# Performance work log

Measured on AMD Instinct MI355X. Metric: run time of the kernel, lower is better.

The kernel has to match this reference:

```python
import jax, jax.numpy as jnp
import numpy as np

N, E, D0, D1, H = 20000, 640000, 64, 32, 64


def setup_inputs() -> dict:
    key = jax.random.key(0)
    ks = jax.random.split(key, 16)
    s = 0.1
    return {
        'feat0e': jax.random.normal(ks[0], (N, D0), jnp.float32),
        'feat1o': jax.random.normal(ks[1], (N, D1, 3), jnp.float32),
        'edge_attr': jax.random.normal(ks[2], (E, H), jnp.float32),
        'pos': jax.random.normal(ks[3], (N, 3), jnp.float32),
        'edge_index': jax.random.randint(ks[4], (2, E), 0, N, jnp.int64),
        # edge_net: FullyConnectedNet([H]*3 -> [H]) with silu
        'W1': jax.random.normal(ks[5], (H, H), jnp.float32) * s,
        'b1': jnp.zeros((H,), jnp.float32),
        'W2': jax.random.normal(ks[6], (H, H), jnp.float32) * s,
        'b2': jnp.zeros((H,), jnp.float32),
        'W3': jax.random.normal(ks[7], (H, H), jnp.float32) * s,
        'b3': jnp.zeros((H,), jnp.float32),
        # tensor-product path weights (internal weights, not shared)
        'w_ss': jax.random.normal(ks[8], (D0, H, D0), jnp.float32) * s,     # 0e x 0e -> 0e
        'w_vv': jax.random.normal(ks[9], (D1, D0), jnp.float32) * s,        # 1o . 1o -> 0e
        'w_sv': jax.random.normal(ks[10], (D0, D1), jnp.float32) * s,       # 0e x 1o -> 1o
        'w_vs': jax.random.normal(ks[11], (D1, H, D1), jnp.float32) * s,    # 1o x 0e -> 1o
        'w_cross': jax.random.normal(ks[12], (D1, D1), jnp.float32) * s,    # 1o x 1o -> 1o (cross)
        # gate: scalars -> per-vector-channel gates
        'Wg': jax.random.normal(ks[13], (D0, D1), jnp.float32) * s,
        'bg': jnp.zeros((D1,), jnp.float32),
    }


def reference(feat0e, feat1o, edge_attr, pos, edge_index,
              W1, b1, W2, b2, W3, b3,
              w_ss, w_vv, w_sv, w_vs, w_cross, Wg, bg):
    src, dst = edge_index[0], edge_index[1]

    # edge MLP (silu)
    h = jax.nn.silu(edge_attr @ W1 + b1)
    h = jax.nn.silu(h @ W2 + b2)
    edge_scalar = h @ W3 + b3                      # [E, H]

    rel_pos = pos[dst] - pos[src]                  # [E, 3]
    s_src = feat0e[src]                            # [E, D0]
    v_src = feat1o[src]                            # [E, D1, 3]

    # equivariant tensor product per edge
    dot_vv = jnp.sum(v_src * rel_pos[:, None, :], axis=-1)          # [E, D1]
    msg0e = (jnp.einsum('ep,eh,pho->eo', s_src, edge_scalar, w_ss)
             + dot_vv @ w_vv)                                        # [E, D0]
    cross_vv = jnp.cross(v_src, rel_pos[:, None, :])                 # [E, D1, 3]
    msg1o = (jnp.einsum('ep,pc,ex->ecx', s_src, w_sv, rel_pos)
             + jnp.einsum('edx,eh,dhc->ecx', v_src, edge_scalar, w_vs)
             + jnp.einsum('edx,dc->ecx', cross_vv, w_cross))          # [E, D1, 3]

    # scatter_mean over destination nodes
    counts = jax.ops.segment_sum(jnp.ones((E,), msg0e.dtype), dst, num_segments=N)
    denom = jnp.maximum(counts, 1.0)
    aggr0e = jax.ops.segment_sum(msg0e, dst, num_segments=N) / denom[:, None]
    aggr1o = jax.ops.segment_sum(msg1o, dst, num_segments=N) / denom[:, None, None]

    # gate + residual
    out0e = jax.nn.silu(aggr0e) + feat0e                              # [N, D0]
    gates = jax.nn.silu(aggr0e @ Wg + bg)                             # [N, D1]
    out1o = aggr1o * gates[:, :, None] + feat1o                       # [N, D1, 3]

    # concat flattened outputs into one array [N, D0 + 3*D1]
    return jnp.concatenate([out0e, out1o.reshape(N, D1 * 3)], axis=-1)
```

## Files before the change

### kernel.cpp

```cpp
#include <hip/hip_runtime.h>


#define NN 20000
#define EE 640000
#define D0 64
#define D1 32
#define HH 64

typedef _Float16 half8 __attribute__((ext_vector_type(8)));
typedef _Float16 half4 __attribute__((ext_vector_type(4)));
typedef float f32x4 __attribute__((ext_vector_type(4)));

__device__ __forceinline__ float silu_f(float x) { return x / (1.0f + __expf(-x)); }
__device__ __forceinline__ _Float16 u2h(unsigned short u) {
    union { unsigned short u; _Float16 h; } c; c.u = u; return c.h;
}
__device__ __forceinline__ unsigned short h2u(_Float16 h) {
    union { unsigned short u; _Float16 h; } c; c.h = h; return c.u;
}
__device__ __forceinline__ half8 pack8(float4 a, float4 b) {
    half8 h;
    h[0]=(_Float16)a.x; h[1]=(_Float16)a.y; h[2]=(_Float16)a.z; h[3]=(_Float16)a.w;
    h[4]=(_Float16)b.x; h[5]=(_Float16)b.y; h[6]=(_Float16)b.z; h[7]=(_Float16)b.w;
    return h;
}

#define OFF_HIST  0ull
#define OFF_RS    81920ull
#define OFF_CUR   163840ull
#define OFF_FLAG  245760ull
#define OFF_SRCA  262144ull
#define OFF_DSTA  2822144ull
#define OFF_PE    5382144ull
#define OFF_WSS   7942144ull
#define OFF_WVS2  8466432ull
#define OFF_WVV   8597504ull
#define OFF_WSV   8601600ull
#define OFF_WX    8605696ull
#define OFF_WMLP  8607744ull
#define OFF_MSG   8632320ull
#define WS_NEED   (8632320ull + 122880000ull)

__global__ void detect_idx_kernel(const int* __restrict__ eidx, int* __restrict__ flag) {
    int odd_nz = 0, even_nz = 0;
    for (int k = 0; k < 64; ++k) {
        if (eidx[2 * k + 1] != 0) odd_nz = 1;
        if (eidx[2 * k] != 0) even_nz = 1;
    }
    *flag = (!odd_nz && even_nz) ? 1 : 0;
}

__global__ __launch_bounds__(256) void hist_kernel(
    const int* __restrict__ eidx, const int* __restrict__ flag,
    int* __restrict__ hist)
{
    const int e = blockIdx.x * 256 + threadIdx.x;
    int d_;
    if (*flag) d_ = (int)((const long long*)eidx)[EE + e];
    else       d_ = eidx[EE + e];
    atomicAdd(hist + d_, 1);
}

__global__ __launch_bounds__(1024) void scan_kernel(
    const int* __restrict__ hist, int* __restrict__ rs, int* __restrict__ cur)
{
    __shared__ int part[1024];
    const int t = threadIdx.x;
    const int base = t * 20;
    int loc[20];
    int tot = 0;
#pragma unroll
    for (int k = 0; k < 20; ++k) {
        int n = base + k;
        int h = (n < NN) ? hist[n] : 0;
        loc[k] = tot; tot += h;
    }
    part[t] = tot;
    __syncthreads();
    for (int off = 1; off < 1024; off <<= 1) {
        int v = (t >= off) ? part[t - off] : 0;
        __syncthreads();
        part[t] += v;
        __syncthreads();
    }
    int excl = part[t] - tot;
#pragma unroll
    for (int k = 0; k < 20; ++k) {
        int n = base + k;
        if (n < NN) { rs[n] = excl + loc[k]; cur[n] = excl + loc[k]; }
    }
    if (t == 1023) rs[NN] = part[1023];
}

__global__ __launch_bounds__(256) void scatter_kernel(
    const int* __restrict__ eidx, const int* __restrict__ flag,
    int* __restrict__ cur, int* __restrict__ srca, int* __restrict__ dsta,
    int* __restrict__ pe)
{
    const int e = blockIdx.x * 256 + threadIdx.x;
    int s_, d_;
    if (*flag) { s_ = (int)((const long long*)eidx)[e]; d_ = (int)((const long long*)eidx)[EE + e]; }
    else       { s_ = eidx[e];                          d_ = eidx[EE + e]; }
    int pos = atomicAdd(cur + d_, 1);
    srca[pos] = s_; dsta[pos] = d_; pe[pos] = e;
}

__global__ __launch_bounds__(256) void prep_kernel(
    const float* __restrict__ wss, const float* __restrict__ wvv,
    const float* __restrict__ wsv, const float* __restrict__ wvs,
    const float* __restrict__ wx,
    const float* __restrict__ W1, const float* __restrict__ W2,
    const float* __restrict__ W3, char* __restrict__ ws)
{
    int id = blockIdx.x * 256 + threadIdx.x;
    if (id >= 43136) return;
    int l = id & 63;
    int l4 = l >> 4, l16 = l & 15;
    half8 o;
    _Float16* dst;
    if (id < 32768) {
        int p = id >> 9; int frag = (id >> 6) & 7;
        int kf = frag >> 2, nf = frag & 3;
#pragma unroll
        for (int j = 0; j < 8; j++) {
            int h = kf * 32 + l4 * 8 + j, oo = nf * 16 + l16;
            o[j] = (_Float16)wss[((size_t)p * 64 + h) * 64 + oo];
        }
        dst = (_Float16*)(ws + OFF_WSS) + (size_t)id * 8;
    } else if (id < 40960) {
        int i = id - 32768;
        int f = i >> 6;
        int chunk = f >> 3, kf = (f >> 2) & 1, nfl = f & 3;
#pragma unroll
        for (int j = 0; j < 8; j++) {
            int h = kf * 32 + l4 * 8 + j;
            int col = chunk * 64 + nfl * 16 + l16;
            int d = col >> 5, c = col & 31;
            o[j] = (_Float16)wvs[((size_t)d * 64 + h) * 32 + c];
        }
        dst = (_Float16*)(ws + OFF_WVS2) + (size_t)i * 8;
    } else if (id < 41216) {
        int i = id - 40960; int nf = i >> 6;
#pragma unroll
        for (int j = 0; j < 8; j++) {
            int d = l4 * 8 + j, oo = nf * 16 + l16;
            o[j] = (_Float16)wvv[d * 64 + oo];
        }
        dst = (_Float16*)(ws + OFF_WVV) + (size_t)i * 8;
    } else if (id < 41472) {
        int i = id - 41216; int frag = i >> 6;
        int kf = frag >> 1, nf = frag & 1;
#pragma unroll
        for (int j = 0; j < 8; j++) {
            int p = kf * 32 + l4 * 8 + j, c = nf * 16 + l16;
            o[j] = (_Float16)wsv[p * 32 + c];
        }
        dst = (_Float16*)(ws + OFF_WSV) + (size_t)i * 8;
    } else if (id < 41600) {
        int i = id - 41472; int nf = i >> 6;
#pragma unroll
        for (int j = 0; j < 8; j++) {
            int d = l4 * 8 + j, c = nf * 16 + l16;
            o[j] = (_Float16)wx[d * 32 + c];
        }
        dst = (_Float16*)(ws + OFF_WX) + (size_t)i * 8;
    } else {
        int i = id - 41600; int f = i >> 6;
        int layer = f >> 3, kf = (f >> 2) & 1, nf = f & 3;
        const float* W = layer == 0 ? W1 : (layer == 1 ? W2 : W3);
#pragma unroll
        for (int j = 0; j < 8; j++) {
            int r = kf * 32 + l4 * 8 + j, cc = nf * 16 + l16;
            o[j] = (_Float16)W[r * 64 + cc];
        }
        dst = (_Float16*)(ws + OFF_WMLP) + (size_t)i * 8;
    }
    *(half8*)dst = o;
}

__device__ __forceinline__ void mlp_wave(
    const float* __restrict__ edge_attr,
    const float* __restrict__ b1, const float* __restrict__ b2,
    const float* __restrict__ b3,
    const char* __restrict__ wsp,
    const int* __restrict__ pel_w,
    unsigned short* __restrict__ xch,
    int lane, half8 esf[4][2])
{
    const int l4 = lane >> 4, l16 = lane & 15;
    const half8* wm = (const half8*)(wsp + OFF_WMLP);

    float bias[3][4];
#pragma unroll
    for (int nf = 0; nf < 4; nf++) {
        bias[0][nf] = b1[nf * 16 + l16];
        bias[1][nf] = b2[nf * 16 + l16];
        bias[2][nf] = b3[nf * 16 + l16];
    }

    half8 af[4][2];
#pragma unroll
    for (int mf = 0; mf < 4; mf++) {
        int e = pel_w[mf * 16 + l16];
        const float* p = edge_attr + (size_t)e * 64 + l4 * 8;
#pragma unroll
        for (int kf = 0; kf < 2; kf++)
            af[mf][kf] = pack8(*(const float4*)(p + kf * 32),
                               *(const float4*)(p + kf * 32 + 4));
    }

#pragma unroll
    for (int layer = 0; layer < 3; ++layer) {
        f32x4 acc[4][4];
#pragma unroll
        for (int mf = 0; mf < 4; mf++)
#pragma unroll
            for (int nf = 0; nf < 4; nf++) acc[mf][nf] = (f32x4){0.f,0.f,0.f,0.f};
#pragma unroll
        for (int kf = 0; kf < 2; kf++)
#pragma unroll
            for (int mf = 0; mf < 4; mf++)
#pragma unroll
                for (int nf = 0; nf < 4; nf++)
                    acc[mf][nf] = __builtin_amdgcn_mfma_f32_16x16x32_f16(
                        af[mf][kf], wm[(layer * 8 + kf * 4 + nf) * 64 + lane],
                        acc[mf][nf], 0, 0, 0);
#pragma unroll
        for (int mf = 0; mf < 4; mf++)
#pragma unroll
            for (int nf = 0; nf < 4; nf++)
#pragma unroll
                for (int reg = 0; reg < 4; reg++) {
                    int row = mf * 16 + l4 * 4 + reg;
                    int col = nf * 16 + l16;
                    float v = acc[mf][nf][reg] + bias[layer][nf];
                    if (layer < 2) v = silu_f(v);
                    xch[row * 64 + (col ^ ((row & 7) << 3))] = h2u((_Float16)v);
                }
        if (layer < 2) {
#pragma unroll
            for (int mf = 0; mf < 4; mf++)
#pragma unroll
                for (int kf = 0; kf < 2; kf++) {
                    int row = mf * 16 + l16;
                    int cs = kf * 32 + l4 * 8;
                    af[mf][kf] = *(const half8*)&xch[row * 64 + (cs ^ ((row & 7) << 3))];
                }
        }
    }
#pragma unroll
    for (int mf = 0; mf < 4; mf++)
#pragma unroll
        for (int kf = 0; kf < 2; kf++) {
            int row = mf * 16 + l16;
            int cs = kf * 32 + l4 * 8;
            esf[mf][kf] = *(const half8*)&xch[row * 64 + (cs ^ ((row & 7) << 3))];
        }
}

__global__ __launch_bounds__(256, 2) void msg0e_kernel(
    const float* __restrict__ feat0e,
    const float* __restrict__ feat1o,
    const float* __restrict__ edge_attr,
    const float* __restrict__ pos,
    const float* __restrict__ b1, const float* __restrict__ b2,
    const float* __restrict__ b3,
    const char* __restrict__ wsp,
    _Float16* __restrict__ msg0)
{
    __shared__ unsigned short st[4][4096];
    __shared__ unsigned short wf[16384];
    __shared__ float rell[4][64][3];
    __shared__ int   srcl[4][64];
    __shared__ int   pel[4][64];

    const int tid = threadIdx.x, w = tid >> 6, lane = tid & 63;
    const int l4 = lane >> 4, l16 = lane & 15;
    const long i0 = (long)blockIdx.x * 256 + w * 64;

    {
        long p = i0 + lane;
        int s_ = ((const int*)(wsp + OFF_SRCA))[p];
        int d_ = ((const int*)(wsp + OFF_DSTA))[p];
        pel[w][lane] = ((const int*)(wsp + OFF_PE))[p];
        srcl[w][lane] = s_;
        rell[w][lane][0] = pos[d_ * 3 + 0] - pos[s_ * 3 + 0];
        rell[w][lane][1] = pos[d_ * 3 + 1] - pos[s_ * 3 + 1];
        rell[w][lane][2] = pos[d_ * 3 + 2] - pos[s_ * 3 + 2];
    }
    __syncthreads();

    half8 esf[4][2];
    mlp_wave(edge_attr, b1, b2, b3, wsp, pel[w], st[w], lane, esf);
    __syncthreads();

#pragma unroll
    for (int r4 = 0; r4 < 4; r4++) {
        int row = r4 * 16 + (lane >> 2);
        int ch = lane & 3;
        const float* sp = feat0e + (size_t)srcl[w][row] * 64 + ch * 16;
        half8 h0 = pack8(*(const float4*)(sp + 0), *(const float4*)(sp + 4));
        half8 h1 = pack8(*(const float4*)(sp + 8), *(const float4*)(sp + 12));
        int r7 = row & 7;
        *(half8*)&st[w][row * 64 + (((ch * 2) ^ r7) * 8)]     = h0;
        *(half8*)&st[w][row * 64 + (((ch * 2 + 1) ^ r7) * 8)] = h1;
    }
    __syncthreads();

    f32x4 acc[4][4];
#pragma unroll
    for (int mf = 0; mf < 4; mf++)
#pragma unroll
        for (int nf = 0; nf < 4; nf++) acc[mf][nf] = (f32x4){0.f, 0.f, 0.f, 0.f};

    const half8* wss_g = (const half8*)(wsp + OFF_WSS);
    half8* wfh = (half8*)wf;
    for (int pc = 0; pc < 16; ++pc) {
        __syncthreads();
#pragma unroll
        for (int q = 0; q < 8; q++)
            wfh[q * 256 + tid] = wss_g[pc * 2048 + q * 256 + tid];
        __syncthreads();
#pragma unroll
        for (int pl = 0; pl < 4; ++pl) {
            const int p = pc * 4 + pl;
            _Float16 sv[4];
#pragma unroll
            for (int mf = 0; mf < 4; mf++) {
                int row = mf * 16 + l16;
                sv[mf] = u2h(st[w][row * 64 + (((p >> 3) ^ (row & 7)) * 8) + (p & 7)]);
            }
#pragma unroll
            for (int kf = 0; kf < 2; kf++) {
                half8 bf[4];
#pragma unroll
                for (int nf = 0; nf < 4; nf++)
                    bf[nf] = wfh[(pl * 8 + kf * 4 + nf) * 64 + lane];
#pragma unroll
                for (int mf = 0; mf < 4; mf++) {
                    half8 a = esf[mf][kf] * sv[mf];
#pragma unroll
                    for (int nf = 0; nf < 4; nf++)
                        acc[mf][nf] = __builtin_amdgcn_mfma_f32_16x16x32_f16(a, bf[nf], acc[mf][nf], 0, 0, 0);
// ... 151 lines not shown
                bsv[kf][nf] = wsvp[(size_t)(kf * 2 + nf) * 64 + lane];
#pragma unroll
        for (int g = 0; g < 4; g++) {
            int erow = g * 16 + l16;
            const float* sp = feat0e + (size_t)srcl[w][erow] * 64 + l4 * 8;
            half8 sf[2];
#pragma unroll
            for (int kf = 0; kf < 2; kf++)
                sf[kf] = pack8(*(const float4*)(sp + kf * 32),
                               *(const float4*)(sp + kf * 32 + 4));
#pragma unroll
            for (int x = 0; x < 3; x++) {
                _Float16 rl = (_Float16)rell[w][erow][x];
#pragma unroll
                for (int kf = 0; kf < 2; kf++) {
                    half8 a = sf[kf] * rl;
#pragma unroll
                    for (int nf = 0; nf < 2; nf++)
                        acc1[g][x][nf] = __builtin_amdgcn_mfma_f32_16x16x32_f16(
                            a, bsv[kf][nf], acc1[g][x][nf], 0, 0, 0);
                }
            }
        }
    }

    {
        half8 bx[2];
        bx[0] = wxp[lane];
        bx[1] = wxp[64 + lane];
#pragma unroll
        for (int g = 0; g < 4; g++) {
            f32x4 cx[3][2];
#pragma unroll
            for (int xp = 0; xp < 3; xp++) {
                half8 av;
#pragma unroll
                for (int j = 0; j < 8; j++)
                    av[j] = u2h(vt[w][((l4 * 8 + j) * 3 + xp) * 64 + g * 16 + l16]);
#pragma unroll
                for (int nf = 0; nf < 2; nf++)
                    cx[xp][nf] = __builtin_amdgcn_mfma_f32_16x16x32_f16(
                        av, bx[nf], (f32x4){0.f,0.f,0.f,0.f}, 0, 0, 0);
            }
            f32x4 r[3];
#pragma unroll
            for (int x = 0; x < 3; x++)
#pragma unroll
                for (int reg = 0; reg < 4; reg++)
                    r[x][reg] = rell[w][g * 16 + l4 * 4 + reg][x];
#pragma unroll
            for (int x = 0; x < 3; x++) {
                const int x1 = (x + 1) % 3, x2 = (x + 2) % 3;
#pragma unroll
                for (int ch = 0; ch < 2; ch++)
                    acc1[g][x][ch] += r[x2] * cx[x1][ch] - r[x1] * cx[x2][ch];
            }
        }
    }

    __syncthreads();
#pragma unroll
    for (int g = 0; g < 4; g++)
#pragma unroll
        for (int reg = 0; reg < 4; reg++) {
            int row = g * 16 + l4 * 4 + reg;
            int sw = (row & 3) << 3;
#pragma unroll
            for (int x = 0; x < 3; x++)
#pragma unroll
                for (int ch = 0; ch < 2; ch++) {
                    int c32 = ch * 16 + l16;
                    vt[w][row * 96 + x * 32 + (c32 ^ sw)] = h2u((_Float16)acc1[g][x][ch][reg]);
                }
        }
#pragma unroll
    for (int tt = 0; tt < 12; tt++) {
        int x = tt >> 2, rem = (tt & 3) * 8;
        int col = x * 32 + (rem ^ ((lane & 3) << 3));
        half8 v = *(const half8*)&vt[w][lane * 96 + col];
        *(half8*)(msg1 + (size_t)(i0 + lane) * 96 + tt * 8) = v;
    }
}

__global__ __launch_bounds__(256) void gather0_kernel(
    const float* __restrict__ feat0e,
    const float* __restrict__ Wg, const float* __restrict__ bg,
    const char* __restrict__ wsp, const _Float16* __restrict__ msg0,
    float* __restrict__ out)
{
    __shared__ float Wgl[2048];
    __shared__ float ag[4][64];
    const int tid = threadIdx.x, w = tid >> 6, lane = tid & 63;
    for (int t = tid; t < 2048; t += 256) Wgl[t] = Wg[t];

    const int n = blockIdx.x * 4 + w;
    const int* rs = (const int*)(wsp + OFF_RS);
    const int i0 = rs[n], i1 = rs[n + 1];
    const int r8 = lane >> 3, c8 = lane & 7;

    float a[8];
#pragma unroll
    for (int j = 0; j < 8; j++) a[j] = 0.f;
    for (int i = i0 + r8; i < i1; i += 8) {
        half8 m = *(const half8*)(msg0 + (size_t)i * 64 + c8 * 8);
#pragma unroll
        for (int j = 0; j < 8; j++) a[j] += (float)m[j];
    }
#pragma unroll
    for (int s = 8; s < 64; s <<= 1)
#pragma unroll
        for (int j = 0; j < 8; j++) a[j] += __shfl_xor(a[j], s);
    if (r8 == 0)
#pragma unroll
        for (int j = 0; j < 8; j++) ag[w][c8 * 8 + j] = a[j];
    __syncthreads();

    const float inv = 1.0f / fmaxf((float)(i1 - i0), 1.0f);
    float av = ag[w][lane] * inv;
    out[(size_t)n * 160 + lane] = silu_f(av) + feat0e[(size_t)n * 64 + lane];

    if (lane < 32) {
        float gs = bg[lane];
#pragma unroll
        for (int p = 0; p < 64; ++p) gs = fmaf(ag[w][p] * inv, Wgl[p * 32 + lane], gs);
        out[(size_t)n * 160 + 64 + lane] = silu_f(gs);
    }
}

__global__ __launch_bounds__(256) void gather1_kernel(
    const float* __restrict__ feat1o,
    const char* __restrict__ wsp, const _Float16* __restrict__ msg1,
    float* __restrict__ out)
{
    __shared__ float ag1[4][96];
    __shared__ float gl[4][32];
    const int tid = threadIdx.x, w = tid >> 6, lane = tid & 63;
    const int n = blockIdx.x * 4 + w;
    const int* rs = (const int*)(wsp + OFF_RS);
    const int i0 = rs[n], i1 = rs[n + 1];

    if (lane < 32) gl[w][lane] = out[(size_t)n * 160 + 64 + lane];

    const int r4 = lane >> 4, c12 = lane & 15;
    float a[8];
#pragma unroll
    for (int j = 0; j < 8; j++) a[j] = 0.f;
    if (c12 < 12)
        for (int i = i0 + r4; i < i1; i += 4) {
            half8 m = *(const half8*)(msg1 + (size_t)i * 96 + c12 * 8);
#pragma unroll
            for (int j = 0; j < 8; j++) a[j] += (float)m[j];
        }
#pragma unroll
    for (int s = 16; s < 64; s <<= 1)
#pragma unroll
        for (int j = 0; j < 8; j++) a[j] += __shfl_xor(a[j], s);
    if (r4 == 0 && c12 < 12)
#pragma unroll
        for (int j = 0; j < 8; j++) ag1[w][c12 * 8 + j] = a[j];
    __syncthreads();

    const float inv = 1.0f / fmaxf((float)(i1 - i0), 1.0f);
#pragma unroll
    for (int t = 0; t < 2; t++) {
        int idx = t * 64 + lane;
        if (idx < 96) {
            int c = idx / 3, x = idx - 3 * c;
            float v = ag1[w][x * 32 + c] * inv * gl[w][c] + feat1o[(size_t)n * 96 + idx];
            out[(size_t)n * 160 + 64 + idx] = v;
        }
    }
}

__global__ __launch_bounds__(256) void edge_kernel_fb(
    const float* __restrict__ feat0e, const float* __restrict__ feat1o,
    const float* __restrict__ edge_attr, const float* __restrict__ pos,
    const int* __restrict__ eidx,
    const float* __restrict__ W1, const float* __restrict__ b1,
    const float* __restrict__ W2, const float* __restrict__ b2,
    const float* __restrict__ W3, const float* __restrict__ b3,
    const float* __restrict__ wss, const float* __restrict__ wvv,
    const float* __restrict__ wsv, const float* __restrict__ wvs,
    const float* __restrict__ wcross,
    const int* __restrict__ i64flag,
    float* __restrict__ out, float* __restrict__ counts)
{
    const int e = blockIdx.x * 256 + threadIdx.x;
    int src, dst;
    if (*i64flag) { src = (int)((const long long*)eidx)[e]; dst = (int)((const long long*)eidx)[EE + e]; }
    else          { src = eidx[e];                          dst = eidx[EE + e]; }
    const float rel0 = pos[dst * 3 + 0] - pos[src * 3 + 0];
    const float rel1 = pos[dst * 3 + 1] - pos[src * 3 + 1];
    const float rel2 = pos[dst * 3 + 2] - pos[src * 3 + 2];
    float h1[HH];
#pragma unroll
    for (int j = 0; j < HH; ++j) h1[j] = b1[j];
    for (int i = 0; i < HH; ++i) {
        float a = edge_attr[(size_t)e * HH + i];
        const float* ww = W1 + i * HH;
#pragma unroll
        for (int j = 0; j < HH; ++j) h1[j] = fmaf(a, ww[j], h1[j]);
    }
#pragma unroll
    for (int j = 0; j < HH; ++j) h1[j] = silu_f(h1[j]);
    float h2[HH];
#pragma unroll
    for (int j = 0; j < HH; ++j) h2[j] = b2[j];
#pragma unroll
    for (int i = 0; i < HH; ++i) {
        float a = h1[i];
        const float* ww = W2 + i * HH;
#pragma unroll
        for (int j = 0; j < HH; ++j) h2[j] = fmaf(a, ww[j], h2[j]);
    }
#pragma unroll
    for (int j = 0; j < HH; ++j) h2[j] = silu_f(h2[j]);
    float es[HH];
#pragma unroll
    for (int j = 0; j < HH; ++j) es[j] = b3[j];
#pragma unroll
    for (int i = 0; i < HH; ++i) {
        float a = h2[i];
        const float* ww = W3 + i * HH;
#pragma unroll
        for (int j = 0; j < HH; ++j) es[j] = fmaf(a, ww[j], es[j]);
    }
    float dotv[D1];
#pragma unroll
    for (int d = 0; d < D1; ++d) {
        float v0 = feat1o[(size_t)src * 96 + d * 3 + 0];
        float v1 = feat1o[(size_t)src * 96 + d * 3 + 1];
        float v2 = feat1o[(size_t)src * 96 + d * 3 + 2];
        dotv[d] = fmaf(v0, rel0, fmaf(v1, rel1, v2 * rel2));
    }
#pragma unroll
    for (int ob = 0; ob < 4; ++ob) {
        const int o0 = ob * 16;
        float acc[16];
#pragma unroll
        for (int j = 0; j < 16; ++j) acc[j] = 0.f;
#pragma unroll
        for (int d = 0; d < D1; ++d) {
            const float* ww = wvv + d * D0 + o0;
#pragma unroll
            for (int j = 0; j < 16; ++j) acc[j] = fmaf(dotv[d], ww[j], acc[j]);
        }
        for (int p = 0; p < D0; ++p) {
            float sval = feat0e[(size_t)src * D0 + p];
            const float* wp = wss + (size_t)p * HH * D0 + o0;
#pragma unroll
            for (int h = 0; h < HH; ++h) {
                float c = sval * es[h];
                const float* ww = wp + h * D0;
#pragma unroll
                for (int j = 0; j < 16; ++j) acc[j] = fmaf(c, ww[j], acc[j]);
            }
        }
        float* obase = out + (size_t)dst * 160 + o0;
#pragma unroll
        for (int j = 0; j < 16; ++j) atomicAdd(obase + j, acc[j]);
    }
    atomicAdd(counts + dst, 1.0f);
    float g[D1];
#pragma unroll
    for (int c = 0; c < D1; ++c) g[c] = 0.f;
    for (int p = 0; p < D0; ++p) {
        float sval = feat0e[(size_t)src * D0 + p];
        const float* ww = wsv + p * D1;
#pragma unroll
        for (int c = 0; c < D1; ++c) g[c] = fmaf(sval, ww[c], g[c]);
    }
    float acc1[D1 * 3];
#pragma unroll
    for (int c = 0; c < D1; ++c) {
        acc1[c * 3 + 0] = g[c] * rel0;
        acc1[c * 3 + 1] = g[c] * rel1;
        acc1[c * 3 + 2] = g[c] * rel2;
    }
    for (int d = 0; d < D1; ++d) {
        float v0 = feat1o[(size_t)src * 96 + d * 3 + 0];
        float v1 = feat1o[(size_t)src * 96 + d * 3 + 1];
        float v2 = feat1o[(size_t)src * 96 + d * 3 + 2];
        float cx0 = fmaf(v1, rel2, -v2 * rel1);
        float cx1 = fmaf(v2, rel0, -v0 * rel2);
        float cx2 = fmaf(v0, rel1, -v1 * rel0);
        const float* wd = wvs + (size_t)d * HH * D1;
        const float* wc = wcross + d * D1;
#pragma unroll
        for (int cb = 0; cb < 2; ++cb) {
            float t[16];
#pragma unroll
            for (int cc = 0; cc < 16; ++cc) t[cc] = 0.f;
#pragma unroll
            for (int h = 0; h < HH; ++h) {
                const float* ww = wd + h * D1 + cb * 16;
                float ev = es[h];
#pragma unroll
                for (int cc = 0; cc < 16; ++cc) t[cc] = fmaf(ev, ww[cc], t[cc]);
            }
#pragma unroll
            for (int cc = 0; cc < 16; ++cc) {
                int c = cb * 16 + cc;
                float tc = t[cc], wcc = wc[c];
                acc1[c * 3 + 0] = fmaf(v0, tc, fmaf(cx0, wcc, acc1[c * 3 + 0]));
                acc1[c * 3 + 1] = fmaf(v1, tc, fmaf(cx1, wcc, acc1[c * 3 + 1]));
                acc1[c * 3 + 2] = fmaf(v2, tc, fmaf(cx2, wcc, acc1[c * 3 + 2]));
            }
        }
    }
    float* obase1 = out + (size_t)dst * 160 + 64;
#pragma unroll
    for (int k = 0; k < D1 * 3; ++k) atomicAdd(obase1 + k, acc1[k]);
}

__global__ __launch_bounds__(256) void node_kernel_fb(
    const float* __restrict__ feat0e,
    const float* __restrict__ feat1o,
    const float* __restrict__ Wg, const float* __restrict__ bg,
    const float* __restrict__ counts,
    float* __restrict__ out)
{
    const int w = threadIdx.x >> 6;
    const int n = blockIdx.x * 4 + w;
    const int lane = threadIdx.x & 63;
    __shared__ float a_lds[4][D0];
    __shared__ float gate_lds[4][D1];

    const float inv = 1.0f / fmaxf(counts[n], 1.0f);
    float a = out[(size_t)n * 160 + lane] * inv;
    a_lds[w][lane] = a;
    __syncthreads();

    out[(size_t)n * 160 + lane] = silu_f(a) + feat0e[(size_t)n * D0 + lane];

    if (lane < D1) {
        float gs = bg[lane];
        for (int p = 0; p < D0; ++p) gs = fmaf(a_lds[w][p], Wg[p * D1 + lane], gs);
        gate_lds[w][lane] = silu_f(gs);
    }
    __syncthreads();

    for (int idx = lane; idx < D1 * 3; idx += 64) {
        int c = idx / 3;
        size_t o = (size_t)n * 160 + 64 + idx;
        out[o] = fmaf(out[o] * inv, gate_lds[w][c], feat1o[(size_t)n * (D1 * 3) + idx]);
    }
}

extern "C" void kernel_launch(void* const* d_in, const int* in_sizes, int n_in,
                              void* d_out, int out_size, void* d_ws, size_t ws_size,
                              hipStream_t stream) {
    const float* feat0e    = (const float*)d_in[0];
    const float* feat1o    = (const float*)d_in[1];
    const float* edge_attr = (const float*)d_in[2];
    const float* pos       = (const float*)d_in[3];
    const int*   eidx      = (const int*)d_in[4];
    const float* W1 = (const float*)d_in[5];
    const float* b1 = (const float*)d_in[6];
    const float* W2 = (const float*)d_in[7];
    const float* b2 = (const float*)d_in[8];
    const float* W3 = (const float*)d_in[9];
    const float* b3 = (const float*)d_in[10];
    const float* wss    = (const float*)d_in[11];
    const float* wvv    = (const float*)d_in[12];
    const float* wsv    = (const float*)d_in[13];
    const float* wvs    = (const float*)d_in[14];
    const float* wcross = (const float*)d_in[15];
    const float* Wg = (const float*)d_in[16];
    const float* bg = (const float*)d_in[17];

    float* out = (float*)d_out;
    char*  ws  = (char*)d_ws;
    int* hist = (int*)(ws + OFF_HIST);
    int* rs   = (int*)(ws + OFF_RS);
    int* cur  = (int*)(ws + OFF_CUR);
    int* flag = (int*)(ws + OFF_FLAG);

    detect_idx_kernel<<<1, 1, 0, stream>>>(eidx, flag);

    if (ws_size >= WS_NEED) {
        int* srca = (int*)(ws + OFF_SRCA);
        int* dsta = (int*)(ws + OFF_DSTA);
        int* pe   = (int*)(ws + OFF_PE);
        _Float16* msg = (_Float16*)(ws + OFF_MSG);

        hipMemsetAsync(ws + OFF_HIST, 0, NN * sizeof(int), stream);
        hist_kernel<<<EE / 256, 256, 0, stream>>>(eidx, flag, hist);
        scan_kernel<<<1, 1024, 0, stream>>>(hist, rs, cur);
        scatter_kernel<<<EE / 256, 256, 0, stream>>>(eidx, flag, cur, srca, dsta, pe);
        prep_kernel<<<169, 256, 0, stream>>>(wss, wvv, wsv, wvs, wcross, W1, W2, W3, ws);

        msg0e_kernel<<<EE / 256, 256, 0, stream>>>(
            feat0e, feat1o, edge_attr, pos, b1, b2, b3, (const char*)ws, msg);
        gather0_kernel<<<NN / 4, 256, 0, stream>>>(
            feat0e, Wg, bg, (const char*)ws, msg, out);
        msg1o_kernel<<<EE / 256, 256, 0, stream>>>(
            feat0e, feat1o, edge_attr, pos, b1, b2, b3, (const char*)ws, msg);
        gather1_kernel<<<NN / 4, 256, 0, stream>>>(
            feat1o, (const char*)ws, msg, out);
    } else {
        float* counts = (float*)(ws + OFF_HIST);
        hipMemsetAsync(d_out, 0, (size_t)out_size * sizeof(float), stream);
        hipMemsetAsync(ws + OFF_HIST, 0, NN * sizeof(float), stream);
        edge_kernel_fb<<<EE / 256, 256, 0, stream>>>(
            feat0e, feat1o, edge_attr, pos, eidx,
            W1, b1, W2, b2, W3, b3, wss, wvv, wsv, wvs, wcross,
            flag, out, counts);
        node_kernel_fb<<<NN / 4, 256, 0, stream>>>(feat0e, feat1o, Wg, bg, counts, out);
    }
}
```

Measured before the change: 767.6 us.

## Precompute per-source tensor-product weights and process edges grouped by source

Edges are re-sorted by source node and padded to 16-edge tiles. Each tile then shares one source, so the per-node tensor feat0e·w_ss (64×64 fp16) can be computed once per node in a new gG kernel. The msg0e kernel now needs only an edge_scalar × G[src] matmul instead of the full three-way contraction, which cuts per-edge MFMA work by roughly the D0 factor. In exchange it adds extra sort/scatter passes, a large G buffer with chunked fallback, padded rows in the edge MLP, and an indirect map lookup in gather0.

```diff
diff --git a/kernel.cpp b/kernel.cpp
--- a/kernel.cpp
+++ b/kernel.cpp
@@ -6,6 +6,8 @@
 #define D0 64
 #define D1 32
 #define HH 64
+#define EPMAX 940032
+#define NTILES 58752
 
 typedef _Float16 half8 __attribute__((ext_vector_type(8)));
 typedef _Float16 half4 __attribute__((ext_vector_type(4)));
@@ -29,6 +31,7 @@
 #define OFF_RS    81920ull
 #define OFF_CUR   163840ull
 #define OFF_FLAG  245760ull
+#define OFF_EPT   245764ull
 #define OFF_SRCA  262144ull
 #define OFF_DSTA  2822144ull
 #define OFF_PE    5382144ull
@@ -39,7 +42,18 @@
 #define OFF_WX    8605696ull
 #define OFF_WMLP  8607744ull
 #define OFF_MSG   8632320ull
-#define WS_NEED   (8632320ull + 122880000ull)
+#define WS_R4_NEED 131512320ull
+#define OFF_WSSG  131512320ull
+#define OFF_OUTD  132036608ull
+#define OFF_PSP   132118528ull
+#define OFF_CURS  132200448ull
+#define OFF_SRCT  132282368ull
+#define OFF_POSOF 132528128ull
+#define OFF_MAP   135088128ull
+#define OFF_DSTP  137648128ull
+#define OFF_PEP   141408256ull
+#define OFF_G     145168384ull
+#define NEED_S(npp) (OFF_G + (unsigned long long)(npp) * 8192ull)
 
 __global__ void detect_idx_kernel(const int* __restrict__ eidx, int* __restrict__ flag) {
     int odd_nz = 0, even_nz = 0;
@@ -50,15 +64,28 @@
     *flag = (!odd_nz && even_nz) ? 1 : 0;
 }
 
+__device__ __forceinline__ void load_sd(const int* eidx, const int* flag, int e,
+                                        int& s_, int& d_) {
+    if (*flag) { s_ = (int)((const long long*)eidx)[e]; d_ = (int)((const long long*)eidx)[EE + e]; }
+    else       { s_ = eidx[e];                          d_ = eidx[EE + e]; }
+}
+
 __global__ __launch_bounds__(256) void hist_kernel(
+    const int* __restrict__ eidx, const int* __restrict__ flag, int* __restrict__ hist)
+{
+    const int e = blockIdx.x * 256 + threadIdx.x;
+    int s_, d_; load_sd(eidx, flag, e, s_, d_);
+    atomicAdd(hist + d_, 1);
+}
+
+__global__ __launch_bounds__(256) void hist2_kernel(
     const int* __restrict__ eidx, const int* __restrict__ flag,
-    int* __restrict__ hist)
+    int* __restrict__ hist, int* __restrict__ outd)
 {
     const int e = blockIdx.x * 256 + threadIdx.x;
-    int d_;
-    if (*flag) d_ = (int)((const long long*)eidx)[EE + e];
-    else       d_ = eidx[EE + e];
+    int s_, d_; load_sd(eidx, flag, e, s_, d_);
     atomicAdd(hist + d_, 1);
+    atomicAdd(outd + s_, 1);
 }
 
 __global__ __launch_bounds__(1024) void scan_kernel(
@@ -92,15 +119,80 @@
     if (t == 1023) rs[NN] = part[1023];
 }
 
-__global__ __launch_bounds__(256) void scatter_kernel(
+__global__ __launch_bounds__(1024) void scanP_kernel(
+    const int* __restrict__ outd, int* __restrict__ psP, int* __restrict__ curS,
+    int* __restrict__ srcT, int* __restrict__ epT)
+{
+    __shared__ int part[1024];
+    const int t = threadIdx.x;
+    const int base = t * 20;
+    int loc[20];
+    int tot = 0;
+#pragma unroll
+    for (int k = 0; k < 20; ++k) {
+        int n = base + k;
+        int p = (n < NN) ? ((outd[n] + 15) & ~15) : 0;
+        loc[k] = tot; tot += p;
+    }
+    part[t] = tot;
+    __syncthreads();
+    for (int off = 1; off < 1024; off <<= 1) {
+        int v = (t >= off) ? part[t - off] : 0;
+        __syncthreads();
+        part[t] += v;
+        __syncthreads();
+    }
+    int excl = part[t] - tot;
+#pragma unroll
+    for (int k = 0; k < 20; ++k) {
+        int n = base + k;
+        if (n < NN) {
+            int start = excl + loc[k];
+            psP[n] = start; curS[n] = start;
+            int p = (outd[n] + 15) & ~15;
+            for (int tt = start >> 4; tt < (start + p) >> 4; ++tt) srcT[tt] = n;
+        }
+    }
+    if (t == 1023) *epT = part[1023] >> 4;
+}
+
+__global__ __launch_bounds__(256) void fillpad_kernel(
+    const int* __restrict__ epT, int* __restrict__ srcT)
+{
+    int t = blockIdx.x * 256 + threadIdx.x;
+    if (t < NTILES && t >= *epT) srcT[t] = NN;
+}
+
+__global__ __launch_bounds__(256) void srcscat_kernel(
+    const int* __restrict__ eidx, const int* __restrict__ flag,
+    int* __restrict__ curS, int* __restrict__ dstP, int* __restrict__ peP,
+    int* __restrict__ posof)
+{
+    const int e = blockIdx.x * 256 + threadIdx.x;
+    int s_, d_; load_sd(eidx, flag, e, s_, d_);
+    int pos = atomicAdd(curS + s_, 1);
+    dstP[pos] = d_; peP[pos] = e; posof[e] = pos;
+}
+
+__global__ __launch_bounds__(256) void dstscat2_kernel(
+    const int* __restrict__ eidx, const int* __restrict__ flag,
+    int* __restrict__ cur, int* __restrict__ srca, int* __restrict__ dsta,
+    int* __restrict__ pe, const int* __restrict__ posof, int* __restrict__ map)
+{
+    const int e = blockIdx.x * 256 + threadIdx.x;
+    int s_, d_; load_sd(eidx, flag, e, s_, d_);
+    int j = atomicAdd(cur + d_, 1);
+    srca[j] = s_; dsta[j] = d_; pe[j] = e;
+    if (map) map[j] = posof[e];
+}
+
+__global__ __launch_bounds__(256) void scatter_r4_kernel(
     const int* __restrict__ eidx, const int* __restrict__ flag,
     int* __restrict__ cur, int* __restrict__ srca, int* __restrict__ dsta,
     int* __restrict__ pe)
 {
     const int e = blockIdx.x * 256 + threadIdx.x;
-    int s_, d_;
-    if (*flag) { s_ = (int)((const long long*)eidx)[e]; d_ = (int)((const long long*)eidx)[EE + e]; }
-    else       { s_ = eidx[e];                          d_ = eidx[EE + e]; }
+    int s_, d_; load_sd(eidx, flag, e, s_, d_);
     int pos = atomicAdd(cur + d_, 1);
     srca[pos] = s_; dsta[pos] = d_; pe[pos] = e;
 }
@@ -110,10 +202,10 @@
     const float* __restrict__ wsv, const float* __restrict__ wvs,
     const float* __restrict__ wx,
     const float* __restrict__ W1, const float* __restrict__ W2,
-    const float* __restrict__ W3, char* __restrict__ ws)
+    const float* __restrict__ W3, char* __restrict__ ws, int maxid)
 {
     int id = blockIdx.x * 256 + threadIdx.x;
-    if (id >= 43136) return;
+    if (id >= maxid) return;
     int l = id & 63;
     int l4 = l >> 4, l16 = l & 15;
     half8 o;
@@ -164,7 +256,7 @@
             o[j] = (_Float16)wx[d * 32 + c];
         }
         dst = (_Float16*)(ws + OFF_WX) + (size_t)i * 8;
-    } else {
+    } else if (id < 43136) {
         int i = id - 41600; int f = i >> 6;
         int layer = f >> 3, kf = (f >> 2) & 1, nf = f & 3;
         const float* W = layer == 0 ? W1 : (layer == 1 ? W2 : W3);
@@ -174,8 +266,62 @@
             o[j] = (_Float16)W[r * 64 + cc];
         }
         dst = (_Float16*)(ws + OFF_WMLP) + (size_t)i * 8;
+    } else {
+        int i = id - 43136;
+        int f = i >> 6;
+        int q = f >> 3, kfp = (f >> 2) & 1, nfp = f & 3;
+#pragma unroll
+        for (int j = 0; j < 8; j++) {
+            int p = kfp * 32 + l4 * 8 + j;
+            int cc = q * 64 + nfp * 16 + l16;
+            int jc = cc & 7, lc = (cc >> 3) & 63, fi = cc >> 9;
+            int kfc = fi >> 2, nfc = fi & 3;
+            int h = kfc * 32 + (lc >> 4) * 8 + jc;
+            int oo = nfc * 16 + (lc & 15);
+            o[j] = (_Float16)wss[((size_t)p * 64 + h) * 64 + oo];
+        }
+        dst = (_Float16*)(ws + OFF_WSSG) + (size_t)i * 8;
     }
     *(half8*)dst = o;
+}
+
+__global__ __launch_bounds__(256, 2) void gG_kernel(
+    const float* __restrict__ feat0e, const char* __restrict__ wsp,
+    int lo, int hi, _Float16* __restrict__ G)
+{
+    const int tid = threadIdx.x, w = tid >> 6, lane = tid & 63;
+    const int l4 = lane >> 4, l16 = lane & 15;
+    const int n0 = lo + blockIdx.x * 64 + w * 16;
+    if (n0 >= hi) return;
+
+    half8 af[2];
+    {
+        int n = n0 + l16; if (n >= NN) n = NN - 1;
+        const float* sp = feat0e + (size_t)n * 64 + l4 * 8;
+        af[0] = pack8(*(const float4*)sp, *(const float4*)(sp + 4));
+        af[1] = pack8(*(const float4*)(sp + 32), *(const float4*)(sp + 36));
+    }
+    const half8* wg = (const half8*)(wsp + OFF_WSSG);
+    for (int q = 0; q < 64; ++q) {
+        f32x4 acc[4];
+#pragma unroll
+        for (int nf = 0; nf < 4; nf++) acc[nf] = (f32x4){0.f,0.f,0.f,0.f};
+#pragma unroll
+        for (int kf = 0; kf < 2; kf++)
+#pragma unroll
+            for (int nf = 0; nf < 4; nf++)
+                acc[nf] = __builtin_amdgcn_mfma_f32_16x16x32_f16(
+                    af[kf], wg[(q * 8 + kf * 4 + nf) * 64 + lane], acc[nf], 0, 0, 0);
+#pragma unroll
+        for (int nf = 0; nf < 4; nf++)
+#pragma unroll
+            for (int reg = 0; reg < 4; reg++) {
+                int n = n0 + l4 * 4 + reg;
+                if (n < hi && n < NN)
+                    G[(size_t)(n - lo) * 4096 + q * 64 + nf * 16 + l16] =
+                        (_Float16)acc[nf][reg];
+            }
+    }
 }
 
 __device__ __forceinline__ void mlp_wave(
@@ -258,7 +404,120 @@
         }
 }
 
-__global__ __launch_bounds__(256, 2) void msg0e_kernel(
+__global__ __launch_bounds__(256, 4) void msg0e_big_kernel(
+    const float* __restrict__ feat1o,
+    const float* __restrict__ edge_attr,
+    const float* __restrict__ pos,
+    const float* __restrict__ b1, const float* __restrict__ b2,
+    const float* __restrict__ b3,
+    const char* __restrict__ wsp,
+    const _Float16* __restrict__ G,
+    int lo, int hi,
+    _Float16* __restrict__ msg0)
+{
+    __shared__ unsigned short st[4][4096];
+    __shared__ float rell[4][64][3];
+    __shared__ int pel[4][64];
+
+    const int tid = threadIdx.x, w = tid >> 6, lane = tid & 63;
+    const int l4 = lane >> 4, l16 = lane & 15;
+    const int i0 = blockIdx.x * 256 + w * 64;
+    const int t0 = i0 >> 4;
+
+    const int* srcT = (const int*)(wsp + OFF_SRCT);
+    int sm[4]; bool act[4]; bool any = false;
+#pragma unroll
+    for (int mf = 0; mf < 4; mf++) {
+        sm[mf] = srcT[t0 + mf];
+        act[mf] = (sm[mf] >= lo && sm[mf] < hi);
+        any = any || act[mf];
+    }
+    if (!any) return;
+
+    {
+        int row = i0 + lane;
+        int my_s = sm[l4];
+        int s_ld = my_s < NN ? my_s : 0;
+        int d_ = ((const int*)(wsp + OFF_DSTP))[row];
+        pel[w][lane] = ((const int*)(wsp + OFF_PEP))[row];
+        rell[w][lane][0] = pos[d_ * 3 + 0] - pos[s_ld * 3 + 0];
+        rell[w][lane][1] = pos[d_ * 3 + 1] - pos[s_ld * 3 + 1];
+        rell[w][lane][2] = pos[d_ * 3 + 2] - pos[s_ld * 3 + 2];
+    }
+
+    half8 esf[4][2];
+    mlp_wave(edge_attr, b1, b2, b3, wsp, pel[w], st[w], lane, esf);
+
+    f32x4 acc[4][4];
+#pragma unroll
+    for (int mf = 0; mf < 4; mf++)
+#pragma unroll
+        for (int nf = 0; nf < 4; nf++) acc[mf][nf] = (f32x4){0.f, 0.f, 0.f, 0.f};
+
+    const half8* Gb = (const half8*)G;
+#pragma unroll
+    for (int mf = 0; mf < 4; mf++) {
+        if (!act[mf]) continue;
+        const half8* gn = Gb + (size_t)(sm[mf] - lo) * 512;
+#pragma unroll
+        for (int kf = 0; kf < 2; kf++)
+#pragma unroll
+            for (int nf = 0; nf < 4; nf++) {
+                half8 bf = gn[(kf * 4 + nf) * 64 + lane];
+                acc[mf][nf] = __builtin_amdgcn_mfma_f32_16x16x32_f16(
+                    esf[mf][kf], bf, acc[mf][nf], 0, 0, 0);
+            }
+    }
+
+    const half8* wvvp = (const half8*)(wsp + OFF_WVV);
+#pragma unroll
+    for (int mf = 0; mf < 4; mf++) {
+        if (!act[mf]) continue;
+        int row = mf * 16 + l16;
+        float r0 = rell[w][row][0], r1 = rell[w][row][1], r2 = rell[w][row][2];
+        const float* vp = feat1o + (size_t)sm[mf] * 96 + l4 * 24;
+        float4 A = *(const float4*)(vp + 0),  B = *(const float4*)(vp + 4);
+        float4 C = *(const float4*)(vp + 8),  D = *(const float4*)(vp + 12);
+        float4 E = *(const float4*)(vp + 16), F = *(const float4*)(vp + 20);
+        half8 dvf;
+        dvf[0] = (_Float16)(A.x * r0 + A.y * r1 + A.z * r2);
+        dvf[1] = (_Float16)(A.w * r0 + B.x * r1 + B.y * r2);
+        dvf[2] = (_Float16)(B.z * r0 + B.w * r1 + C.x * r2);
+        dvf[3] = (_Float16)(C.y * r0 + C.z * r1 + C.w * r2);
+        dvf[4] = (_Float16)(D.x * r0 + D.y * r1 + D.z * r2);
+        dvf[5] = (_Float16)(D.w * r0 + E.x * r1 + E.y * r2);
+        dvf[6] = (_Float16)(E.z * r0 + E.w * r1 + F.x * r2);
+        dvf[7] = (_Float16)(F.y * r0 + F.z * r1 + F.w * r2);
+#pragma unroll
+        for (int nf = 0; nf < 4; nf++)
+            acc[mf][nf] = __builtin_amdgcn_mfma_f32_16x16x32_f16(
+                dvf, wvvp[nf * 64 + lane], acc[mf][nf], 0, 0, 0);
+    }
+
+#pragma unroll
+    for (int mf = 0; mf < 4; mf++) {
+        if (!act[mf]) continue;
+#pragma unroll
+        for (int nf = 0; nf < 4; nf++)
+#pragma unroll
+            for (int reg = 0; reg < 4; reg++) {
+                int row = mf * 16 + l4 * 4 + reg;
+                int col = nf * 16 + l16;
+                st[w][row * 64 + (col ^ ((row & 7) << 3))] =
+                    h2u((_Float16)acc[mf][nf][reg]);
+            }
+    }
+#pragma unroll
+    for (int t = 0; t < 8; t++) {
+        if (!act[t >> 1]) continue;
+        int row = t * 8 + (lane >> 3);
+        int c8 = lane & 7;
+        half8 v = *(const half8*)&st[w][row * 64 + ((c8 * 8) ^ ((row & 7) << 3))];
+        *(half8*)(msg0 + (size_t)(i0 + row) * 64 + c8 * 8) = v;
+    }
+}
+
+__global__ __launch_bounds__(256, 2) void msg0e_r4_kernel(
     const float* __restrict__ feat0e,
     const float* __restrict__ feat1o,
     const float* __restrict__ edge_attr,
@@ -576,7 +835,7 @@
     }
 }
 
-__global__ __launch_bounds__(256) void gather0_kernel(
+__global__ __launch_bounds__(256) void gather0_r4_kernel(
     const float* __restrict__ feat0e,
     const float* __restrict__ Wg, const float* __restrict__ bg,
     const char* __restrict__ wsp, const _Float16* __restrict__ msg0,
@@ -597,6 +856,53 @@
     for (int j = 0; j < 8; j++) a[j] = 0.f;
     for (int i = i0 + r8; i < i1; i += 8) {
         half8 m = *(const half8*)(msg0 + (size_t)i * 64 + c8 * 8);
+#pragma unroll
+        for (int j = 0; j < 8; j++) a[j] += (float)m[j];
+    }
+#pragma unroll
+    for (int s = 8; s < 64; s <<= 1)
+#pragma unroll
+        for (int j = 0; j < 8; j++) a[j] += __shfl_xor(a[j], s);
+    if (r8 == 0)
+#pragma unroll
+        for (int j = 0; j < 8; j++) ag[w][c8 * 8 + j] = a[j];
+    __syncthreads();
+
+    const float inv = 1.0f / fmaxf((float)(i1 - i0), 1.0f);
+    float av = ag[w][lane] * inv;
+    out[(size_t)n * 160 + lane] = silu_f(av) + feat0e[(size_t)n * 64 + lane];
+
+    if (lane < 32) {
+        float gs = bg[lane];
+#pragma unroll
+        for (int p = 0; p < 64; ++p) gs = fmaf(ag[w][p] * inv, Wgl[p * 32 + lane], gs);
+        out[(size_t)n * 160 + 64 + lane] = silu_f(gs);
+    }
+}
+
+__global__ __launch_bounds__(256) void gather0_big_kernel(
+    const float* __restrict__ feat0e,
+    const float* __restrict__ Wg, const float* __restrict__ bg,
+    const char* __restrict__ wsp, const _Float16* __restrict__ msg0,
+    float* __restrict__ out)
+{
+    __shared__ float Wgl[2048];
+    __shared__ float ag[4][64];
+    const int tid = threadIdx.x, w = tid >> 6, lane = tid & 63;
+    for (int t = tid; t < 2048; t += 256) Wgl[t] = Wg[t];
+
+    const int n = blockIdx.x * 4 + w;
+    const int* rs = (const int*)(wsp + OFF_RS);
+    const int* map = (const int*)(wsp + OFF_MAP);
+    const int i0 = rs[n], i1 = rs[n + 1];
+    const int r8 = lane >> 3, c8 = lane & 7;
+
+    float a[8];
+#pragma unroll
+    for (int j = 0; j < 8; j++) a[j] = 0.f;
+    for (int i = i0 + r8; i < i1; i += 8) {
+        int row = map[i];
+        half8 m = *(const half8*)(msg0 + (size_t)row * 64 + c8 * 8);
 #pragma unroll
         for (int j = 0; j < 8; j++) a[j] += (float)m[j];
     }
@@ -663,181 +969,6 @@
             float v = ag1[w][x * 32 + c] * inv * gl[w][c] + feat1o[(size_t)n * 96 + idx];
             out[(size_t)n * 160 + 64 + idx] = v;
         }
-    }
-}
-
-__global__ __launch_bounds__(256) void edge_kernel_fb(
-    const float* __restrict__ feat0e, const float* __restrict__ feat1o,
-    const float* __restrict__ edge_attr, const float* __restrict__ pos,
-    const int* __restrict__ eidx,
-    const float* __restrict__ W1, const float* __restrict__ b1,
-    const float* __restrict__ W2, const float* __restrict__ b2,
-    const float* __restrict__ W3, const float* __restrict__ b3,
-    const float* __restrict__ wss, const float* __restrict__ wvv,
-    const float* __restrict__ wsv, const float* __restrict__ wvs,
-    const float* __restrict__ wcross,
-    const int* __restrict__ i64flag,
-    float* __restrict__ out, float* __restrict__ counts)
-{
-    const int e = blockIdx.x * 256 + threadIdx.x;
-    int src, dst;
-    if (*i64flag) { src = (int)((const long long*)eidx)[e]; dst = (int)((const long long*)eidx)[EE + e]; }
-    else          { src = eidx[e];                          dst = eidx[EE + e]; }
-    const float rel0 = pos[dst * 3 + 0] - pos[src * 3 + 0];
-    const float rel1 = pos[dst * 3 + 1] - pos[src * 3 + 1];
-    const float rel2 = pos[dst * 3 + 2] - pos[src * 3 + 2];
-    float h1[HH];
-#pragma unroll
-    for (int j = 0; j < HH; ++j) h1[j] = b1[j];
-    for (int i = 0; i < HH; ++i) {
-        float a = edge_attr[(size_t)e * HH + i];
-        const float* ww = W1 + i * HH;
-#pragma unroll
-        for (int j = 0; j < HH; ++j) h1[j] = fmaf(a, ww[j], h1[j]);
-    }
-#pragma unroll
-    for (int j = 0; j < HH; ++j) h1[j] = silu_f(h1[j]);
-    float h2[HH];
-#pragma unroll
-    for (int j = 0; j < HH; ++j) h2[j] = b2[j];
-#pragma unroll
-    for (int i = 0; i < HH; ++i) {
-        float a = h1[i];
-        const float* ww = W2 + i * HH;
-#pragma unroll
-        for (int j = 0; j < HH; ++j) h2[j] = fmaf(a, ww[j], h2[j]);
-    }
-#pragma unroll
-    for (int j = 0; j < HH; ++j) h2[j] = silu_f(h2[j]);
-    float es[HH];
-#pragma unroll
-    for (int j = 0; j < HH; ++j) es[j] = b3[j];
-#pragma unroll
-    for (int i = 0; i < HH; ++i) {
-        float a = h2[i];
-        const float* ww = W3 + i * HH;
-#pragma unroll
-        for (int j = 0; j < HH; ++j) es[j] = fmaf(a, ww[j], es[j]);
-    }
-    float dotv[D1];
-#pragma unroll
-    for (int d = 0; d < D1; ++d) {
-        float v0 = feat1o[(size_t)src * 96 + d * 3 + 0];
-        float v1 = feat1o[(size_t)src * 96 + d * 3 + 1];
-        float v2 = feat1o[(size_t)src * 96 + d * 3 + 2];
-        dotv[d] = fmaf(v0, rel0, fmaf(v1, rel1, v2 * rel2));
-    }
-#pragma unroll
-    for (int ob = 0; ob < 4; ++ob) {
-        const int o0 = ob * 16;
-        float acc[16];
-#pragma unroll
-        for (int j = 0; j < 16; ++j) acc[j] = 0.f;
-#pragma unroll
-        for (int d = 0; d < D1; ++d) {
-            const float* ww = wvv + d * D0 + o0;
-#pragma unroll
-            for (int j = 0; j < 16; ++j) acc[j] = fmaf(dotv[d], ww[j], acc[j]);
-        }
-        for (int p = 0; p < D0; ++p) {
-            float sval = feat0e[(size_t)src * D0 + p];
-            const float* wp = wss + (size_t)p * HH * D0 + o0;
-#pragma unroll
-            for (int h = 0; h < HH; ++h) {
-                float c = sval * es[h];
-                const float* ww = wp + h * D0;
-#pragma unroll
-                for (int j = 0; j < 16; ++j) acc[j] = fmaf(c, ww[j], acc[j]);
-            }
-        }
-        float* obase = out + (size_t)dst * 160 + o0;
-#pragma unroll
-        for (int j = 0; j < 16; ++j) atomicAdd(obase + j, acc[j]);
-    }
-    atomicAdd(counts + dst, 1.0f);
-    float g[D1];
-#pragma unroll
-    for (int c = 0; c < D1; ++c) g[c] = 0.f;
-    for (int p = 0; p < D0; ++p) {
-        float sval = feat0e[(size_t)src * D0 + p];
-        const float* ww = wsv + p * D1;
-#pragma unroll
-        for (int c = 0; c < D1; ++c) g[c] = fmaf(sval, ww[c], g[c]);
-    }
-    float acc1[D1 * 3];
-#pragma unroll
-    for (int c = 0; c < D1; ++c) {
-        acc1[c * 3 + 0] = g[c] * rel0;
-        acc1[c * 3 + 1] = g[c] * rel1;
-        acc1[c * 3 + 2] = g[c] * rel2;
-    }
-    for (int d = 0; d < D1; ++d) {
-        float v0 = feat1o[(size_t)src * 96 + d * 3 + 0];
-        float v1 = feat1o[(size_t)src * 96 + d * 3 + 1];
-        float v2 = feat1o[(size_t)src * 96 + d * 3 + 2];
-        float cx0 = fmaf(v1, rel2, -v2 * rel1);
-        float cx1 = fmaf(v2, rel0, -v0 * rel2);
-        float cx2 = fmaf(v0, rel1, -v1 * rel0);
-        const float* wd = wvs + (size_t)d * HH * D1;
-        const float* wc = wcross + d * D1;
-#pragma unroll
-        for (int cb = 0; cb < 2; ++cb) {
-            float t[16];
-#pragma unroll
-            for (int cc = 0; cc < 16; ++cc) t[cc] = 0.f;
-#pragma unroll
-            for (int h = 0; h < HH; ++h) {
-                const float* ww = wd + h * D1 + cb * 16;
-                float ev = es[h];
-#pragma unroll
-                for (int cc = 0; cc < 16; ++cc) t[cc] = fmaf(ev, ww[cc], t[cc]);
-            }
-#pragma unroll
-            for (int cc = 0; cc < 16; ++cc) {
-                int c = cb * 16 + cc;
-                float tc = t[cc], wcc = wc[c];
-                acc1[c * 3 + 0] = fmaf(v0, tc, fmaf(cx0, wcc, acc1[c * 3 + 0]));
-                acc1[c * 3 + 1] = fmaf(v1, tc, fmaf(cx1, wcc, acc1[c * 3 + 1]));
-                acc1[c * 3 + 2] = fmaf(v2, tc, fmaf(cx2, wcc, acc1[c * 3 + 2]));
-            }
-        }
-    }
-    float* obase1 = out + (size_t)dst * 160 + 64;
-#pragma unroll
-    for (int k = 0; k < D1 * 3; ++k) atomicAdd(obase1 + k, acc1[k]);
-}
-
-__global__ __launch_bounds__(256) void node_kernel_fb(
-    const float* __restrict__ feat0e,
-    const float* __restrict__ feat1o,
-    const float* __restrict__ Wg, const float* __restrict__ bg,
-    const float* __restrict__ counts,
-    float* __restrict__ out)
-{
-    const int w = threadIdx.x >> 6;
-    const int n = blockIdx.x * 4 + w;
-    const int lane = threadIdx.x & 63;
-    __shared__ float a_lds[4][D0];
-    __shared__ float gate_lds[4][D1];
-
-    const float inv = 1.0f / fmaxf(counts[n], 1.0f);
-    float a = out[(size_t)n * 160 + lane] * inv;
-    a_lds[w][lane] = a;
-    __syncthreads();
-
-    out[(size_t)n * 160 + lane] = silu_f(a) + feat0e[(size_t)n * D0 + lane];
-
-    if (lane < D1) {
-        float gs = bg[lane];
-        for (int p = 0; p < D0; ++p) gs = fmaf(a_lds[w][p], Wg[p * D1 + lane], gs);
-        gate_lds[w][lane] = silu_f(gs);
-    }
-    __syncthreads();
-
-    for (int idx = lane; idx < D1 * 3; idx += 64) {
-        int c = idx / 3;
-        size_t o = (size_t)n * 160 + 64 + idx;
-        out[o] = fmaf(out[o] * inv, gate_lds[w][c], feat1o[(size_t)n * (D1 * 3) + idx]);
     }
 }
 
@@ -869,37 +1000,73 @@
     int* rs   = (int*)(ws + OFF_RS);
     int* cur  = (int*)(ws + OFF_CUR);
     int* flag = (int*)(ws + OFF_FLAG);
+    int* srca = (int*)(ws + OFF_SRCA);
+    int* dsta = (int*)(ws + OFF_DSTA);
+    int* pe   = (int*)(ws + OFF_PE);
+    _Float16* msg = (_Float16*)(ws + OFF_MSG);
 
     detect_idx_kernel<<<1, 1, 0, stream>>>(eidx, flag);
-
-    if (ws_size >= WS_NEED) {
-        int* srca = (int*)(ws + OFF_SRCA);
-        int* dsta = (int*)(ws + OFF_DSTA);
-        int* pe   = (int*)(ws + OFF_PE);
-        _Float16* msg = (_Float16*)(ws + OFF_MSG);
-
-        hipMemsetAsync(ws + OFF_HIST, 0, NN * sizeof(int), stream);
-        hist_kernel<<<EE / 256, 256, 0, stream>>>(eidx, flag, hist);
+    hipMemsetAsync(ws + OFF_HIST, 0, NN * sizeof(int), stream);
+
+    int S = 0;
+    if (ws_size >= NEED_S(20000)) S = 1;
+    else if (ws_size >= NEED_S(10000)) S = 2;
+    else if (ws_size >= NEED_S(5000))  S = 4;
+    else if (ws_size >= NEED_S(2500))  S = 8;
+
+    if (S > 0) {
+        int* outd  = (int*)(ws + OFF_OUTD);
+        int* psP   = (int*)(ws + OFF_PSP);
+        int* curS  = (int*)(ws + OFF_CURS);
+        int* srcT  = (int*)(ws + OFF_SRCT);
+        int* epT   = (int*)(ws + OFF_EPT);
+        int* posof = (int*)(ws + OFF_POSOF);
+        int* map   = (int*)(ws + OFF_MAP);
+        int* dstP  = (int*)(ws + OFF_DSTP);
+        int* peP   = (int*)(ws + OFF_PEP);
+        _Float16* G = (_Float16*)(ws + OFF_G);
+
+        hipMemsetAsync(ws + OFF_OUTD, 0, NN * sizeof(int), stream);
+        hipMemsetAsync(ws + OFF_DSTP, 0, 2 * EPMAX * sizeof(int), stream);
+
+        hist2_kernel<<<EE / 256, 256, 0, stream>>>(eidx, flag, hist, outd);
         scan_kernel<<<1, 1024, 0, stream>>>(hist, rs, cur);
-        scatter_kernel<<<EE / 256, 256, 0, stream>>>(eidx, flag, cur, srca, dsta, pe);
-        prep_kernel<<<169, 256, 0, stream>>>(wss, wvv, wsv, wvs, wcross, W1, W2, W3, ws);
-
-        msg0e_kernel<<<EE / 256, 256, 0, stream>>>(
-            feat0e, feat1o, edge_attr, pos, b1, b2, b3, (const char*)ws, msg);
-        gather0_kernel<<<NN / 4, 256, 0, stream>>>(
+        scanP_kernel<<<1, 1024, 0, stream>>>(outd, psP, curS, srcT, epT);
+        fillpad_kernel<<<(NTILES + 255) / 256, 256, 0, stream>>>(epT, srcT);
+        srcscat_kernel<<<EE / 256, 256, 0, stream>>>(eidx, flag, curS, dstP, peP, posof);
+        dstscat2_kernel<<<EE / 256, 256, 0, stream>>>(eidx, flag, cur, srca, dsta, pe,
+                                                      posof, map);
+        prep_kernel<<<(75904 + 255) / 256, 256, 0, stream>>>(
+            wss, wvv, wsv, wvs, wcross, W1, W2, W3, ws, 75904);
+
+        const int npp = (NN + S - 1) / S;
+        for (int s = 0; s < S; ++s) {
+            int lo = s * npp;
+            int hi = lo + npp; if (hi > NN) hi = NN;
+            gG_kernel<<<(hi - lo + 63) / 64, 256, 0, stream>>>(
+                feat0e, (const char*)ws, lo, hi, G);
+            msg0e_big_kernel<<<EPMAX / 256, 256, 0, stream>>>(
+                feat1o, edge_attr, pos, b1, b2, b3, (const char*)ws, G, lo, hi, msg);
+        }
+        gather0_big_kernel<<<NN / 4, 256, 0, stream>>>(
             feat0e, Wg, bg, (const char*)ws, msg, out);
         msg1o_kernel<<<EE / 256, 256, 0, stream>>>(
             feat0e, feat1o, edge_attr, pos, b1, b2, b3, (const char*)ws, msg);
         gather1_kernel<<<NN / 4, 256, 0, stream>>>(
             feat1o, (const char*)ws, msg, out);
     } else {
-        float* counts = (float*)(ws + OFF_HIST);
-        hipMemsetAsync(d_out, 0, (size_t)out_size * sizeof(float), stream);
-        hipMemsetAsync(ws + OFF_HIST, 0, NN * sizeof(float), stream);
-        edge_kernel_fb<<<EE / 256, 256, 0, stream>>>(
-            feat0e, feat1o, edge_attr, pos, eidx,
-            W1, b1, W2, b2, W3, b3, wss, wvv, wsv, wvs, wcross,
-            flag, out, counts);
-        node_kernel_fb<<<NN / 4, 256, 0, stream>>>(feat0e, feat1o, Wg, bg, counts, out);
-    }
-}
+        hist_kernel<<<EE / 256, 256, 0, stream>>>(eidx, flag, hist);
+        scan_kernel<<<1, 1024, 0, stream>>>(hist, rs, cur);
+        scatter_r4_kernel<<<EE / 256, 256, 0, stream>>>(eidx, flag, cur, srca, dsta, pe);
+        prep_kernel<<<(43136 + 255) / 256, 256, 0, stream>>>(
+            wss, wvv, wsv, wvs, wcross, W1, W2, W3, ws, 43136);
+        msg0e_r4_kernel<<<EE / 256, 256, 0, stream>>>(
+            feat0e, feat1o, edge_attr, pos, b1, b2, b3, (const char*)ws, msg);
+        gather0_r4_kernel<<<NN / 4, 256, 0, stream>>>(
+            feat0e, Wg, bg, (const char*)ws, msg, out);
+        msg1o_kernel<<<EE / 256, 256, 0, stream>>>(
+            feat0e, feat1o, edge_attr, pos, b1, b2, b3, (const char*)ws, msg);
+        gather1_kernel<<<NN / 4, 256, 0, stream>>>(
+            feat1o, (const char*)ws, msg, out);
+    }
+}
```

Measured after the change: 1.060 ms. 38.0% more time.
